# Kernel optimization log

Hardware: AMD Instinct MI355X
Metric: run time of the kernel (lower is better)

## Reference

```python
import jax, jax.numpy as jnp
import numpy as np
import math

NUM_HEADS = 16
HEAD_SIZE = 64
BLOCK = 64          # SLA block size for pooled block scores / sparse selection
TOPK_RATIO = 0.1    # fraction of KV blocks attended per query block


def setup_inputs() -> dict:
    key = jax.random.key(0)
    kq, kk, kv = jax.random.split(key, 3)
    B, S, HD = 2, 4096, NUM_HEADS * HEAD_SIZE
    return {
        "query": jax.random.normal(kq, (B, S, HD), dtype=jnp.float32),
        "key": jax.random.normal(kk, (B, S, HD), dtype=jnp.float32),
        "value": jax.random.normal(kv, (B, S, HD), dtype=jnp.float32),
    }


def _sla_attention(q, k, v):
    # q, k, v: (B, H, S, D). Block-topk sparse attention (SLA-style):
    # mean-pool q/k per block, score blocks, keep top-k key blocks per
    # query block, gather only those K/V blocks, softmax over them.
    B, H, S, D = q.shape
    Nb = S // BLOCK
    scale = 1.0 / math.sqrt(D)

    qb = q.reshape(B, H, Nb, BLOCK, D)
    kb = k.reshape(B, H, Nb, BLOCK, D)
    vb = v.reshape(B, H, Nb, BLOCK, D)

    q_pool = qb.mean(axis=3)  # (B,H,Nb,D)
    k_pool = kb.mean(axis=3)  # (B,H,Nb,D)
    block_scores = jnp.einsum("bhid,bhjd->bhij", q_pool, k_pool) * scale

    K = max(1, int(math.ceil(TOPK_RATIO * Nb)))
    _, idx = jax.lax.top_k(block_scores, K)  # (B,H,Nb,K) selected key blocks

    # Gather selected key/value blocks: (B,H,Nb,K,BLOCK,D)
    gather_idx = idx[..., None, None]
    k_sel = jnp.take_along_axis(kb[:, :, None], gather_idx, axis=3)
    v_sel = jnp.take_along_axis(vb[:, :, None], gather_idx, axis=3)

    # Per-query-block scores over the K*BLOCK selected keys
    scores = jnp.einsum("bhnqd,bhnkjd->bhnqkj", qb, k_sel) * scale
    scores = scores.reshape(B, H, Nb, BLOCK, K * BLOCK)
    probs = jax.nn.softmax(scores, axis=-1)

    v_flat = v_sel.reshape(B, H, Nb, K * BLOCK, D)
    out = jnp.einsum("bhnqk,bhnkd->bhnqd", probs, v_flat)
    return out.reshape(B, H, S, D)


def reference(query, key, value):
    B, S, HD = query.shape
    H, D = NUM_HEADS, HEAD_SIZE
    # b s (h d) -> b h s d
    q = query.reshape(B, S, H, D).transpose(0, 2, 1, 3)
    k = key.reshape(B, S, H, D).transpose(0, 2, 1, 3)
    v = value.reshape(B, S, H, D).transpose(0, 2, 1, 3)
    out = _sla_attention(q, k, v)  # (B,H,S,D)
    # b h s d -> b s (h d)
    return out.transpose(0, 2, 1, 3).reshape(B, S, HD)
```

## Files before the change

kernel.cpp:

```cpp
#include <hip/hip_runtime.h>

constexpr int Bn = 2;
constexpr int Sn = 4096;
constexpr int Hh = 16;
constexpr int Dn = 64;
constexpr int HD = 1024;
constexpr int NB = 64;
constexpr int KS = 7;

typedef _Float16 f16x8 __attribute__((ext_vector_type(8)));
typedef _Float16 f16x4 __attribute__((ext_vector_type(4)));
typedef _Float16 f16x2 __attribute__((ext_vector_type(2)));
typedef __fp16   hf2   __attribute__((ext_vector_type(2)));
typedef float    f32x4 __attribute__((ext_vector_type(4)));

static __device__ __forceinline__ f16x8 cvt8(float4 a, float4 b) {
    f16x8 r;
    r[0] = (_Float16)a.x; r[1] = (_Float16)a.y;
    r[2] = (_Float16)a.z; r[3] = (_Float16)a.w;
    r[4] = (_Float16)b.x; r[5] = (_Float16)b.y;
    r[6] = (_Float16)b.z; r[7] = (_Float16)b.w;
    return r;
}

static __device__ __forceinline__ f16x4 pk4(float a, float b, float c, float d) {
    hf2 lo = __builtin_amdgcn_cvt_pkrtz(a, b);
    hf2 hi = __builtin_amdgcn_cvt_pkrtz(c, d);
    f16x2 l2 = __builtin_bit_cast(f16x2, lo);
    f16x2 h2 = __builtin_bit_cast(f16x2, hi);
    f16x4 r;
    r[0] = l2[0]; r[1] = l2[1]; r[2] = h2[0]; r[3] = h2[1];
    return r;
}

__global__ __launch_bounds__(64) void sla_pool(const float* __restrict__ Q,
                                               const float* __restrict__ K,
                                               float* __restrict__ qpool,
                                               float* __restrict__ kpool) {
    int bid  = blockIdx.x;
    int b    = bid / (Hh * NB);
    int rem  = bid % (Hh * NB);
    int h    = rem / NB;
    int nb   = rem % NB;
    int tid  = threadIdx.x;
    int quad = tid >> 4;
    int dq   = (tid & 15) << 2;

    const float* qb = Q + ((size_t)b * Sn + (size_t)nb * 64) * HD + h * Dn + dq;
    const float* kb = K + ((size_t)b * Sn + (size_t)nb * 64) * HD + h * Dn + dq;

    double sq[4] = {0, 0, 0, 0}, sk[4] = {0, 0, 0, 0};
    #pragma unroll
    for (int i = 0; i < 16; ++i) {
        size_t off = (size_t)(quad + i * 4) * HD;
        float4 x = *(const float4*)(qb + off);
        float4 y = *(const float4*)(kb + off);
        sq[0] += x.x; sq[1] += x.y; sq[2] += x.z; sq[3] += x.w;
        sk[0] += y.x; sk[1] += y.y; sk[2] += y.z; sk[3] += y.w;
    }
    #pragma unroll
    for (int j = 0; j < 4; ++j) {
        sq[j] += __shfl_xor(sq[j], 16); sq[j] += __shfl_xor(sq[j], 32);
        sk[j] += __shfl_xor(sk[j], 16); sk[j] += __shfl_xor(sk[j], 32);
    }
    if (quad == 0) {
        float4 oq, ok;
        oq.x = (float)(sq[0] * (1.0 / 64.0)); oq.y = (float)(sq[1] * (1.0 / 64.0));
        oq.z = (float)(sq[2] * (1.0 / 64.0)); oq.w = (float)(sq[3] * (1.0 / 64.0));
        ok.x = (float)(sk[0] * (1.0 / 64.0)); ok.y = (float)(sk[1] * (1.0 / 64.0));
        ok.z = (float)(sk[2] * (1.0 / 64.0)); ok.w = (float)(sk[3] * (1.0 / 64.0));
        *(float4*)(qpool + (size_t)bid * 64 + dq) = oq;
        *(float4*)(kpool + (size_t)bid * 64 + dq) = ok;
    }
}

__global__ __launch_bounds__(64) void sla_topk(const float* __restrict__ qpool,
                                               const float* __restrict__ kpool,
                                               int* __restrict__ topk) {
    int bid = blockIdx.x;
    int bh  = bid / NB;
    int j   = threadIdx.x;

    const float* qp = qpool + (size_t)bid * 64;
    const float* kp = kpool + ((size_t)bh * NB + j) * 64;
    double s = 0.0;
    #pragma unroll 8
    for (int d = 0; d < 64; ++d) s += (double)qp[d] * (double)kp[d];

    double v  = s;
    int   idx = j;
    #pragma unroll
    for (int it = 0; it < KS; ++it) {
        double bv = v; int bi = idx;
        #pragma unroll
        for (int off = 1; off < 64; off <<= 1) {
            double ov = __shfl_xor(bv, off);
            int    oi = __shfl_xor(bi, off);
            if (ov > bv || (ov == bv && oi < bi)) { bv = ov; bi = oi; }
        }
        if (j == 0) topk[(size_t)bid * KS + it] = bi;
        if (idx == bi) v = -1e300;
    }
}

__global__ __launch_bounds__(64) void sla_attn(const float* __restrict__ Q,
                                               const float* __restrict__ K,
                                               const float* __restrict__ V,
                                               const int* __restrict__ topk,
                                               float* __restrict__ O) {
    __shared__ float Kl[4096];
    __shared__ float Vl[4096];

    int raw = blockIdx.x;
    int bid = (raw & 7) * 256 + (raw >> 3);

    int b   = bid / (Hh * NB);
    int rem = bid % (Hh * NB);
    int h   = rem / NB;
    int nb  = rem % NB;

    int lane = threadIdx.x & 63;
    int c    = lane & 15;
    int g    = lane >> 4;

    const int* tkp = topk + (size_t)bid * KS;
    int j0 = __builtin_amdgcn_readfirstlane(tkp[0]);

    const float* kbase = K + (size_t)b * Sn * HD + h * Dn;
    const float* vbase = V + (size_t)b * Sn * HD + h * Dn;
    const float* qbase = Q + ((size_t)b * Sn + (size_t)nb * 64) * HD + h * Dn;

    int cx[4];
    #pragma unroll
    for (int j = 0; j < 4; ++j) cx[j] = (c ^ j) << 2;

    #define ISSUE16(basep, blk, ldsarr) do {                                         \
        const float* _bp = (basep) + ((size_t)(blk) * 64 + g) * HD;                  \
        _Pragma("unroll")                                                            \
        for (int _ch = 0; _ch < 16; ++_ch) {                                         \
            const float* _src = _bp + (size_t)_ch * 4 * HD + cx[_ch & 3];            \
            __builtin_amdgcn_global_load_lds(                                        \
                (const __attribute__((address_space(1))) void*)_src,                 \
                (__attribute__((address_space(3))) void*)&(ldsarr)[_ch * 256],       \
                16, 0, 0);                                                           \
        }                                                                            \
    } while (0)

    float4 qraw[4][2][2];
    #pragma unroll
    for (int f = 0; f < 4; ++f) {
        const float* qrow = qbase + (size_t)(f * 16 + c) * HD;
        #pragma unroll
        for (int s2 = 0; s2 < 2; ++s2) {
            qraw[f][s2][0] = *(const float4*)(qrow + s2 * 32 + g * 8);
            qraw[f][s2][1] = *(const float4*)(qrow + s2 * 32 + g * 8 + 4);
        }
    }
    ISSUE16(kbase, j0, Kl);
    ISSUE16(vbase, j0, Vl);

    const float QS = 0.18033688f;
    f16x8 qf[4][2];
    #pragma unroll
    for (int f = 0; f < 4; ++f) {
        #pragma unroll
        for (int s2 = 0; s2 < 2; ++s2) {
            float4 a0 = qraw[f][s2][0], a1 = qraw[f][s2][1];
            f16x8 q;
            q[0] = (_Float16)(a0.x * QS); q[1] = (_Float16)(a0.y * QS);
            q[2] = (_Float16)(a0.z * QS); q[3] = (_Float16)(a0.w * QS);
            q[4] = (_Float16)(a1.x * QS); q[5] = (_Float16)(a1.y * QS);
            q[6] = (_Float16)(a1.z * QS); q[7] = (_Float16)(a1.w * QS);
            qf[f][s2] = q;
        }
    }

    f32x4 oacc[4][4];
    #pragma unroll
    for (int f = 0; f < 4; ++f)
        #pragma unroll
        for (int tt = 0; tt < 4; ++tt) oacc[f][tt] = f32x4{0.f, 0.f, 0.f, 0.f};
    float rl[4] = {0.f, 0.f, 0.f, 0.f};

    int o1 = (g << 3) ^ ((c >> 2) << 2);
    int vc = (g << 8) + (c ^ (g << 2));

    for (int kb = 0; kb < KS; ++kb) {
        int kn = (kb + 1 < KS) ? kb + 1 : 0;
        int jn = __builtin_amdgcn_readfirstlane(tkp[kn]);

        asm volatile("s_waitcnt vmcnt(16)" ::: "memory");

        f32x4 sacc[4][4];
        #pragma unroll
        for (int f = 0; f < 4; ++f)
            #pragma unroll
            for (int t = 0; t < 4; ++t) sacc[f][t] = f32x4{0.f, 0.f, 0.f, 0.f};
        #pragma unroll
        for (int t = 0; t < 4; ++t) {
            int rb = (t * 16 + c) * 64;
            float4 ka0 = *(const float4*)&Kl[rb + o1];
            float4 ka1 = *(const float4*)&Kl[rb + (o1 ^ 4)];
            float4 kb0 = *(const float4*)&Kl[rb + 32 + o1];
            float4 kb1 = *(const float4*)&Kl[rb + 32 + (o1 ^ 4)];
            f16x8 a0 = cvt8(ka0, ka1);
            f16x8 a1 = cvt8(kb0, kb1);
            #pragma unroll
            for (int f = 0; f < 4; ++f) {
                sacc[f][t] = __builtin_amdgcn_mfma_f32_16x16x32_f16(a0, qf[f][0], sacc[f][t], 0, 0, 0);
                sacc[f][t] = __builtin_amdgcn_mfma_f32_16x16x32_f16(a1, qf[f][1], sacc[f][t], 0, 0, 0);
            }
        }
        asm volatile("s_waitcnt lgkmcnt(0)" ::: "memory");
        if (kb + 1 < KS) ISSUE16(kbase, jn, Kl);

        f16x4 e4[4][4];
        #pragma unroll
        for (int f = 0; f < 4; ++f) {
            #pragma unroll
            for (int t = 0; t < 4; ++t) {
                float x0 = __builtin_amdgcn_exp2f(sacc[f][t][0]);
                float x1 = __builtin_amdgcn_exp2f(sacc[f][t][1]);
                float x2 = __builtin_amdgcn_exp2f(sacc[f][t][2]);
                float x3 = __builtin_amdgcn_exp2f(sacc[f][t][3]);
                rl[f] += (x0 + x1) + (x2 + x3);
                e4[f][t] = pk4(x0, x1, x2, x3);
            }
        }

        if (kb + 1 < KS) asm volatile("s_waitcnt vmcnt(16)" ::: "memory");
        else             asm volatile("s_waitcnt vmcnt(0)"  ::: "memory");

        #pragma unroll
        for (int tt = 0; tt < 4; ++tt) {
            #pragma unroll
            for (int t = 0; t < 4; ++t) {
                int base = t * 1024 + tt * 16 + vc;
                float v0 = Vl[base];
                float v1 = Vl[base + 64];
                float v2 = Vl[base + 128];
                float v3 = Vl[base + 192];
                f16x4 va = pk4(v0, v1, v2, v3);
                #pragma unroll
                for (int f = 0; f < 4; ++f)
                    oacc[f][tt] = __builtin_amdgcn_mfma_f32_16x16x16f16(va, e4[f][t], oacc[f][tt], 0, 0, 0);
            }
        }
        asm volatile("s_waitcnt lgkmcnt(0)" ::: "memory");
        if (kb + 1 < KS) ISSUE16(vbase, jn, Vl);
    }

    #pragma unroll
    for (int f = 0; f < 4; ++f) {
        rl[f] += __shfl_xor(rl[f], 16);
        rl[f] += __shfl_xor(rl[f], 32);
    }
    #pragma unroll
    for (int f = 0; f < 4; ++f) {
        float inv = 1.0f / rl[f];
        float* orow = O + ((size_t)b * Sn + (size_t)nb * 64 + f * 16 + c) * HD + h * Dn;
        #pragma unroll
        for (int tt = 0; tt < 4; ++tt) {
            float4 o4;
            o4.x = oacc[f][tt][0] * inv; o4.y = oacc[f][tt][1] * inv;
            o4.z = oacc[f][tt][2] * inv; o4.w = oacc[f][tt][3] * inv;
            *(float4*)(orow + tt * 16 + g * 4) = o4;
        }
    }
    #undef ISSUE16
}

extern "C" void kernel_launch(void* const* d_in, const int* in_sizes, int n_in,
                              void* d_out, int out_size, void* d_ws, size_t ws_size,
                              hipStream_t stream) {
    const float* Q = (const float*)d_in[0];
    const float* K = (const float*)d_in[1];
    const float* V = (const float*)d_in[2];
    float* O = (float*)d_out;

    float* qpool = (float*)d_ws;
    float* kpool = qpool + (size_t)Bn * Hh * NB * Dn;
    int*   topk  = (int*)(kpool + (size_t)Bn * Hh * NB * Dn);

    dim3 grid(Bn * Hh * NB);
    sla_pool<<<grid, 64, 0, stream>>>(Q, K, qpool, kpool);
    sla_topk<<<grid, 64, 0, stream>>>(qpool, kpool, topk);
    sla_attn<<<grid, 64, 0, stream>>>(Q, K, V, topk, O);
}
```

Baseline: 74.24 us.

## Pre-convert K/V to swizzled fp16 blocks and transposed V before sparse attention

A new prep kernel replaces the pooling kernel. It computes the q/k block means and also writes K as swizzled fp16 blocks and V as transposed, swizzled fp16 blocks into the workspace. The attention kernel then loads half as many bytes per selected block into LDS and skips the per-use fp32-to-fp16 conversions. It also reads all top-k indices up front and raises wave priority around the MFMA loops. The cost is an extra full pass over V and larger workspace traffic. The old path is kept as a fallback when the workspace is too small.

```diff
diff --git a/kernel.cpp b/kernel.cpp
--- a/kernel.cpp
+++ b/kernel.cpp
@@ -31,6 +31,88 @@
     f16x4 r;
     r[0] = l2[0]; r[1] = l2[1]; r[2] = h2[0]; r[3] = h2[1];
     return r;
+}
+
+__global__ __launch_bounds__(256) void sla_prep(const float* __restrict__ Q,
+                                                const float* __restrict__ K,
+                                                const float* __restrict__ V,
+                                                float* __restrict__ qpool,
+                                                float* __restrict__ kpool,
+                                                _Float16* __restrict__ Kh,
+                                                _Float16* __restrict__ Vt) {
+    __shared__ float Tl[64][68];
+
+    int bid = blockIdx.x;
+    int b   = bid / (Hh * NB);
+    int rem = bid % (Hh * NB);
+    int h   = rem / NB;
+    int nb  = rem % NB;
+
+    int t  = threadIdx.x;
+    int r  = t >> 2;
+    int q4 = t & 3;
+    int dq = q4 << 4;
+
+    const size_t rowbase = ((size_t)b * Sn + (size_t)nb * 64) * HD + h * Dn;
+    const float* qp = Q + rowbase + (size_t)r * HD + dq;
+    const float* kp = K + rowbase + (size_t)r * HD + dq;
+    const float* vp = V + rowbase + (size_t)r * HD + dq;
+
+    float4 qx[4], kx[4], vx[4];
+    #pragma unroll
+    for (int i = 0; i < 4; ++i) qx[i] = *(const float4*)(qp + i * 4);
+    #pragma unroll
+    for (int i = 0; i < 4; ++i) kx[i] = *(const float4*)(kp + i * 4);
+    #pragma unroll
+    for (int i = 0; i < 4; ++i) vx[i] = *(const float4*)(vp + i * 4);
+
+    #pragma unroll
+    for (int i = 0; i < 4; ++i) *(float4*)&Tl[r][dq + i * 4] = qx[i];
+    __syncthreads();
+    if (t < 64) {
+        double s = 0.0;
+        #pragma unroll 8
+        for (int rr = 0; rr < 64; ++rr) s += (double)Tl[rr][t];
+        qpool[(size_t)bid * 64 + t] = (float)(s * (1.0 / 64.0));
+    }
+    __syncthreads();
+
+    {
+        _Float16* khrow = Kh + ((size_t)bid * 64 + r) * 64;
+        int s0 = ((q4 << 1) + 0) ^ (r & 7);
+        int s1 = ((q4 << 1) + 1) ^ (r & 7);
+        *(f16x8*)(khrow + (s0 << 3)) = cvt8(kx[0], kx[1]);
+        *(f16x8*)(khrow + (s1 << 3)) = cvt8(kx[2], kx[3]);
+    }
+    #pragma unroll
+    for (int i = 0; i < 4; ++i) *(float4*)&Tl[r][dq + i * 4] = kx[i];
+    __syncthreads();
+    if (t < 64) {
+        double s = 0.0;
+        #pragma unroll 8
+        for (int rr = 0; rr < 64; ++rr) s += (double)Tl[rr][t];
+        kpool[(size_t)bid * 64 + t] = (float)(s * (1.0 / 64.0));
+    }
+    __syncthreads();
+
+    #pragma unroll
+    for (int i = 0; i < 4; ++i) *(float4*)&Tl[r][dq + i * 4] = vx[i];
+    __syncthreads();
+    {
+        int d  = r;
+        _Float16* vtrow = Vt + ((size_t)bid * 64 + d) * 64;
+        #pragma unroll
+        for (int si = 0; si < 4; ++si) {
+            int s  = (q4 << 2) + si;
+            int ch = s ^ (d & 15);
+            f16x4 v4;
+            v4[0] = (_Float16)Tl[(ch << 2) + 0][d];
+            v4[1] = (_Float16)Tl[(ch << 2) + 1][d];
+            v4[2] = (_Float16)Tl[(ch << 2) + 2][d];
+            v4[3] = (_Float16)Tl[(ch << 2) + 3][d];
+            *(f16x4*)(vtrow + (s << 2)) = v4;
+        }
+    }
 }
 
 __global__ __launch_bounds__(64) void sla_pool(const float* __restrict__ Q,
@@ -103,13 +185,13 @@
     }
 }
 
-__global__ __launch_bounds__(64) void sla_attn(const float* __restrict__ Q,
-                                               const float* __restrict__ K,
-                                               const float* __restrict__ V,
-                                               const int* __restrict__ topk,
-                                               float* __restrict__ O) {
-    __shared__ float Kl[4096];
-    __shared__ float Vl[4096];
+__global__ __launch_bounds__(64) void sla_attn16(const float* __restrict__ Q,
+                                                 const _Float16* __restrict__ Kh,
+                                                 const _Float16* __restrict__ Vt,
+                                                 const int* __restrict__ topk,
+                                                 float* __restrict__ O) {
+    __shared__ _Float16 Kl[4096];
+    __shared__ _Float16 Vl[4096];
 
     int raw = blockIdx.x;
     int bid = (raw & 7) * 256 + (raw >> 3);
@@ -123,6 +205,165 @@
     int c    = lane & 15;
     int g    = lane >> 4;
 
+    int jidx[KS];
+    {
+        const int* tkp = topk + (size_t)bid * KS;
+        #pragma unroll
+        for (int i = 0; i < KS; ++i)
+            jidx[i] = __builtin_amdgcn_readfirstlane(tkp[i]);
+    }
+
+    const size_t bhbase = (size_t)(bid - nb) * 4096;
+    const float* qbase  = Q + ((size_t)b * Sn + (size_t)nb * 64) * HD + h * Dn;
+
+    auto ISSUE8 = [&](const _Float16* blkbase, _Float16* ldsbase) {
+        #pragma unroll
+        for (int ch = 0; ch < 8; ++ch) {
+            const _Float16* src = blkbase + ch * 512 + lane * 8;
+            __builtin_amdgcn_global_load_lds(
+                (const __attribute__((address_space(1))) void*)src,
+                (__attribute__((address_space(3))) void*)(ldsbase + ch * 512),
+                16, 0, 0);
+        }
+    };
+
+    float4 qraw[4][2][2];
+    #pragma unroll
+    for (int f = 0; f < 4; ++f) {
+        const float* qrow = qbase + (size_t)(f * 16 + c) * HD;
+        #pragma unroll
+        for (int s2 = 0; s2 < 2; ++s2) {
+            qraw[f][s2][0] = *(const float4*)(qrow + s2 * 32 + g * 8);
+            qraw[f][s2][1] = *(const float4*)(qrow + s2 * 32 + g * 8 + 4);
+        }
+    }
+    ISSUE8(Kh + bhbase + (size_t)jidx[0] * 4096, Kl);
+    ISSUE8(Vt + bhbase + (size_t)jidx[0] * 4096, Vl);
+
+    const float QS = 0.18033688f;
+    f16x8 qf[4][2];
+    #pragma unroll
+    for (int f = 0; f < 4; ++f) {
+        #pragma unroll
+        for (int s2 = 0; s2 < 2; ++s2) {
+            float4 a0 = qraw[f][s2][0], a1 = qraw[f][s2][1];
+            f16x8 q;
+            q[0] = (_Float16)(a0.x * QS); q[1] = (_Float16)(a0.y * QS);
+            q[2] = (_Float16)(a0.z * QS); q[3] = (_Float16)(a0.w * QS);
+            q[4] = (_Float16)(a1.x * QS); q[5] = (_Float16)(a1.y * QS);
+            q[6] = (_Float16)(a1.z * QS); q[7] = (_Float16)(a1.w * QS);
+            qf[f][s2] = q;
+        }
+    }
+
+    f32x4 oacc[4][4];
+    #pragma unroll
+    for (int f = 0; f < 4; ++f)
+        #pragma unroll
+        for (int tt = 0; tt < 4; ++tt) oacc[f][tt] = f32x4{0.f, 0.f, 0.f, 0.f};
+    float rl[4] = {0.f, 0.f, 0.f, 0.f};
+
+    int ks0 = (g ^ (c & 7)) << 3;
+
+    #pragma unroll
+    for (int kb = 0; kb < KS; ++kb) {
+        asm volatile("s_waitcnt vmcnt(8)" ::: "memory");
+
+        f32x4 sacc[4][4];
+        #pragma unroll
+        for (int f = 0; f < 4; ++f)
+            #pragma unroll
+            for (int t = 0; t < 4; ++t) sacc[f][t] = f32x4{0.f, 0.f, 0.f, 0.f};
+        __builtin_amdgcn_s_setprio(1);
+        #pragma unroll
+        for (int t = 0; t < 4; ++t) {
+            int rb = (t * 16 + c) * 64;
+            f16x8 a0 = *(const f16x8*)&Kl[rb + ks0];
+            f16x8 a1 = *(const f16x8*)&Kl[rb + (ks0 ^ 32)];
+            #pragma unroll
+            for (int f = 0; f < 4; ++f) {
+                sacc[f][t] = __builtin_amdgcn_mfma_f32_16x16x32_f16(a0, qf[f][0], sacc[f][t], 0, 0, 0);
+                sacc[f][t] = __builtin_amdgcn_mfma_f32_16x16x32_f16(a1, qf[f][1], sacc[f][t], 0, 0, 0);
+            }
+        }
+        __builtin_amdgcn_s_setprio(0);
+
+        asm volatile("s_waitcnt lgkmcnt(0)" ::: "memory");
+        if (kb + 1 < KS) ISSUE8(Kh + bhbase + (size_t)jidx[kb + 1] * 4096, Kl);
+
+        f16x4 e4[4][4];
+        #pragma unroll
+        for (int f = 0; f < 4; ++f) {
+            #pragma unroll
+            for (int t = 0; t < 4; ++t) {
+                float x0 = __builtin_amdgcn_exp2f(sacc[f][t][0]);
+                float x1 = __builtin_amdgcn_exp2f(sacc[f][t][1]);
+                float x2 = __builtin_amdgcn_exp2f(sacc[f][t][2]);
+                float x3 = __builtin_amdgcn_exp2f(sacc[f][t][3]);
+                rl[f] += (x0 + x1) + (x2 + x3);
+                e4[f][t] = pk4(x0, x1, x2, x3);
+            }
+        }
+
+        if (kb + 1 < KS) asm volatile("s_waitcnt vmcnt(8)" ::: "memory");
+        else             asm volatile("s_waitcnt vmcnt(0)" ::: "memory");
+
+        __builtin_amdgcn_s_setprio(1);
+        #pragma unroll
+        for (int tt = 0; tt < 4; ++tt) {
+            #pragma unroll
+            for (int t = 0; t < 4; ++t) {
+                f16x4 va = *(const f16x4*)&Vl[(tt * 16 + c) * 64 + (((4 * t + g) ^ c) << 2)];
+                #pragma unroll
+                for (int f = 0; f < 4; ++f)
+                    oacc[f][tt] = __builtin_amdgcn_mfma_f32_16x16x16f16(va, e4[f][t], oacc[f][tt], 0, 0, 0);
+            }
+        }
+        __builtin_amdgcn_s_setprio(0);
+
+        asm volatile("s_waitcnt lgkmcnt(0)" ::: "memory");
+        if (kb + 1 < KS) ISSUE8(Vt + bhbase + (size_t)jidx[kb + 1] * 4096, Vl);
+    }
+
+    #pragma unroll
+    for (int f = 0; f < 4; ++f) {
+        rl[f] += __shfl_xor(rl[f], 16);
+        rl[f] += __shfl_xor(rl[f], 32);
+    }
+    #pragma unroll
+    for (int f = 0; f < 4; ++f) {
+        float inv = 1.0f / rl[f];
+        float* orow = O + ((size_t)b * Sn + (size_t)nb * 64 + f * 16 + c) * HD + h * Dn;
+        #pragma unroll
+        for (int tt = 0; tt < 4; ++tt) {
+            float4 o4;
+            o4.x = oacc[f][tt][0] * inv; o4.y = oacc[f][tt][1] * inv;
+            o4.z = oacc[f][tt][2] * inv; o4.w = oacc[f][tt][3] * inv;
+            *(float4*)(orow + tt * 16 + g * 4) = o4;
+        }
+    }
+}
+
+__global__ __launch_bounds__(64) void sla_attn32(const float* __restrict__ Q,
+                                                 const float* __restrict__ K,
+                                                 const float* __restrict__ V,
+                                                 const int* __restrict__ topk,
+                                                 float* __restrict__ O) {
+    __shared__ float Kl[4096];
+    __shared__ float Vl[4096];
+
+    int raw = blockIdx.x;
+    int bid = (raw & 7) * 256 + (raw >> 3);
+
+    int b   = bid / (Hh * NB);
+    int rem = bid % (Hh * NB);
+    int h   = rem / NB;
+    int nb  = rem % NB;
+
+    int lane = threadIdx.x & 63;
+    int c    = lane & 15;
+    int g    = lane >> 4;
+
     const int* tkp = topk + (size_t)bid * KS;
     int j0 = __builtin_amdgcn_readfirstlane(tkp[0]);
 
@@ -134,7 +375,7 @@
     #pragma unroll
     for (int j = 0; j < 4; ++j) cx[j] = (c ^ j) << 2;
 
-    #define ISSUE16(basep, blk, ldsarr) do {                                         \
+    #define ISSUE16F(basep, blk, ldsarr) do {                                        \
         const float* _bp = (basep) + ((size_t)(blk) * 64 + g) * HD;                  \
         _Pragma("unroll")                                                            \
         for (int _ch = 0; _ch < 16; ++_ch) {                                         \
@@ -156,8 +397,8 @@
             qraw[f][s2][1] = *(const float4*)(qrow + s2 * 32 + g * 8 + 4);
         }
     }
-    ISSUE16(kbase, j0, Kl);
-    ISSUE16(vbase, j0, Vl);
+    ISSUE16F(kbase, j0, Kl);
+    ISSUE16F(vbase, j0, Vl);
 
     const float QS = 0.18033688f;
     f16x8 qf[4][2];
@@ -212,7 +453,7 @@
             }
         }
         asm volatile("s_waitcnt lgkmcnt(0)" ::: "memory");
-        if (kb + 1 < KS) ISSUE16(kbase, jn, Kl);
+        if (kb + 1 < KS) ISSUE16F(kbase, jn, Kl);
 
         f16x4 e4[4][4];
         #pragma unroll
@@ -247,7 +488,7 @@
             }
         }
         asm volatile("s_waitcnt lgkmcnt(0)" ::: "memory");
-        if (kb + 1 < KS) ISSUE16(vbase, jn, Vl);
+        if (kb + 1 < KS) ISSUE16F(vbase, jn, Vl);
     }
 
     #pragma unroll
@@ -267,7 +508,7 @@
             *(float4*)(orow + tt * 16 + g * 4) = o4;
         }
     }
-    #undef ISSUE16
+    #undef ISSUE16F
 }
 
 extern "C" void kernel_launch(void* const* d_in, const int* in_sizes, int n_in,
@@ -278,12 +519,26 @@
     const float* V = (const float*)d_in[2];
     float* O = (float*)d_out;
 
+    constexpr size_t NPOOL = (size_t)Bn * Hh * NB * Dn;
+    constexpr size_t NTOPK = (size_t)Bn * Hh * NB * KS;
+    constexpr size_t NBLK  = (size_t)Bn * Hh * NB * 64 * 64;
+
     float* qpool = (float*)d_ws;
-    float* kpool = qpool + (size_t)Bn * Hh * NB * Dn;
-    int*   topk  = (int*)(kpool + (size_t)Bn * Hh * NB * Dn);
+    float* kpool = qpool + NPOOL;
+    int*   topk  = (int*)(kpool + NPOOL);
+    _Float16* Kh = (_Float16*)(topk + NTOPK);
+    _Float16* Vt = Kh + NBLK;
+
+    size_t need = 2 * NPOOL * 4 + NTOPK * 4 + 2 * NBLK * 2;
 
     dim3 grid(Bn * Hh * NB);
-    sla_pool<<<grid, 64, 0, stream>>>(Q, K, qpool, kpool);
-    sla_topk<<<grid, 64, 0, stream>>>(qpool, kpool, topk);
-    sla_attn<<<grid, 64, 0, stream>>>(Q, K, V, topk, O);
-}
+    if (ws_size >= need) {
+        sla_prep<<<grid, 256, 0, stream>>>(Q, K, V, qpool, kpool, Kh, Vt);
+        sla_topk<<<grid, 64, 0, stream>>>(qpool, kpool, topk);
+        sla_attn16<<<grid, 64, 0, stream>>>(Q, Kh, Vt, topk, O);
+    } else {
+        sla_pool<<<grid, 64, 0, stream>>>(Q, K, qpool, kpool);
+        sla_topk<<<grid, 64, 0, stream>>>(qpool, kpool, topk);
+        sla_attn32<<<grid, 64, 0, stream>>>(Q, K, V, topk, O);
+    }
+}
```

Result: slower. 162.4 us (+118.8%).
